# Performance work log

Measured on AMD Instinct MI355X. Metric: run time of the kernel, lower is better.

The kernel has to match this reference:

```python
import jax, jax.numpy as jnp
import numpy as np

A = 32          # num input capsule types
PSIZE = 16      # caps_size (pose matrix 4x4)
MD = 4          # mat_dim = sqrt(caps_size)
NCLS = 10       # output capsules / classes
KF = 5          # routing kernel (final_shape)
KK = KF * KF
KKA = KK * A
ITERS = 3
FINAL_LAMBDA = 0.01
EPS = 1e-12
LN2PI = float(np.log(2.0 * np.pi))
BN_EPS = 1e-5


def unfold(x, k, stride, pad):
    # torch.nn.functional.unfold: [b,C,h,w] -> [b, C*k*k, L], (c, kh, kw) channel-major
    b, c, h, w = x.shape
    if pad:
        x = jnp.pad(x, ((0, 0), (0, 0), (pad, pad), (pad, pad)))
    oh = (h + 2 * pad - k) // stride + 1
    ow = (w + 2 * pad - k) // stride + 1
    cols = jnp.stack([
        jnp.stack([x[:, :, i:i + stride * oh:stride, j:j + stride * ow:stride]
                   for j in range(k)], axis=3)
        for i in range(k)], axis=2)          # [b, c, k, k, oh, ow]
    return cols.reshape(b, c * k * k, oh * ow)


def conv3x3(x, w):
    return jax.lax.conv_general_dilated(x, w, (1, 1), [(1, 1), (1, 1)],
                                        dimension_numbers=('NCHW', 'OIHW', 'NCHW'))


def bn_inf(x, g, b, m, v):
    scale = g / jnp.sqrt(v + BN_EPS)
    return (x - m[None, :, None, None]) * scale[None, :, None, None] + b[None, :, None, None]


def em_routing(a_in, pose, W, beta_u, beta_a):
    b = a_in.shape[0]
    # pose votes
    pu = unfold(pose, KF, 1, 0)                     # [b, A*PSIZE*KK, l]
    l = pu.shape[-1]
    pu = pu.reshape(b, A, PSIZE, KK, l).transpose(0, 4, 3, 1, 2).reshape(b, l, KKA, PSIZE)
    pm = pu.reshape(b, l, KKA, MD, MD)[:, :, :, None]        # [b,l,kkA,1,md,md]
    v = jnp.matmul(pm, W)                                    # [b,l,kkA,B,md,md]
    v = v.reshape(b, l, KKA, NCLS, PSIZE)
    # activations
    au = unfold(a_in, KF, 1, 0).reshape(b, A, KK, l).transpose(0, 3, 2, 1).reshape(b, l, KKA)
    r = jnp.ones((b, l, KKA, NCLS, 1), v.dtype)
    a_out = mu = None
    for i in range(ITERS):
        lam = FINAL_LAMBDA * (1.0 - 0.95 ** (i + 1))
        # M-step
        rw = r * au[:, :, :, None, None]
        r_sum = rw.sum(axis=2, keepdims=True)                # [b,l,1,B,1]
        coeff = rw / (r_sum + EPS)
        mu = (coeff * v).sum(axis=2, keepdims=True)          # [b,l,1,B,psize]
        sigma_sq = (coeff * (v - mu) ** 2).sum(axis=2, keepdims=True) + EPS
        r_s = r_sum[:, :, 0]                                 # [b,l,B,1]
        sig = sigma_sq[:, :, 0]                              # [b,l,B,psize]
        cost_h = (beta_u + 0.5 * jnp.log(sig)) * r_s         # log(sqrt(s)) = 0.5*log(s)
        a_out = jax.nn.sigmoid(lam * (beta_a - cost_h.sum(axis=3)))   # [b,l,B]
        if i < ITERS - 1:
            # E-step (note: log(sigma_sq * ln2pi) as in original code)
            ln_p = (-0.5 * jnp.sum(jnp.log(sigma_sq * LN2PI), axis=-1)
                    - jnp.sum((v - mu) ** 2 / (2.0 * sigma_sq), axis=-1))   # [b,l,kkA,B]
            ln_ap = ln_p + jnp.log(a_out)[:, :, None, :]
            r = jax.nn.softmax(ln_ap, axis=-1)[..., None]
    oh = int(np.floor(np.sqrt(l)))
    pose_out = mu[:, :, 0].reshape(b, l, -1).transpose(0, 2, 1).reshape(b, -1, oh, oh)
    a_map = a_out.transpose(0, 2, 1).reshape(b, -1, oh, oh)
    return a_map, pose_out


def setup_inputs():
    key = jax.random.key(0)
    ks = jax.random.split(key, 14)
    batch = 256
    x = jax.random.normal(ks[0], (batch, 512, 5, 5), jnp.float32)
    w_a = jax.random.normal(ks[1], (A, 512, 3, 3), jnp.float32) * 0.02
    w_pose = jax.random.normal(ks[2], (A * PSIZE, 512, 3, 3), jnp.float32) * 0.02
    bn_a_g = 1.0 + 0.1 * jax.random.normal(ks[3], (A,), jnp.float32)
    bn_a_b = 0.1 * jax.random.normal(ks[4], (A,), jnp.float32)
    bn_a_m = 0.1 * jax.random.normal(ks[5], (A,), jnp.float32)
    bn_a_v = jax.random.uniform(ks[6], (A,), jnp.float32, 0.5, 1.5)
    C2 = A * PSIZE
    bn_p_g = 1.0 + 0.1 * jax.random.normal(ks[7], (C2,), jnp.float32)
    bn_p_b = 0.1 * jax.random.normal(ks[8], (C2,), jnp.float32)
    bn_p_m = 0.1 * jax.random.normal(ks[9], (C2,), jnp.float32)
    bn_p_v = jax.random.uniform(ks[10], (C2,), jnp.float32, 0.5, 1.5)
    W = jax.random.normal(ks[11], (KKA, NCLS, MD, MD), jnp.float32) * 0.25
    beta_u = jnp.zeros((1, 1, NCLS, 1), jnp.float32)
    beta_a = jnp.zeros((1, 1, NCLS), jnp.float32)
    return {"x": x, "w_a": w_a, "w_pose": w_pose,
            "bn_a_g": bn_a_g, "bn_a_b": bn_a_b, "bn_a_m": bn_a_m, "bn_a_v": bn_a_v,
            "bn_p_g": bn_p_g, "bn_p_b": bn_p_b, "bn_p_m": bn_p_m, "bn_p_v": bn_p_v,
            "W": W, "beta_u": beta_u, "beta_a": beta_a}


def reference(x, w_a, w_pose, bn_a_g, bn_a_b, bn_a_m, bn_a_v,
              bn_p_g, bn_p_b, bn_p_m, bn_p_v, W, beta_u, beta_a):
    a = jax.nn.sigmoid(bn_inf(conv3x3(x, w_a), bn_a_g, bn_a_b, bn_a_m, bn_a_v))
    pose = bn_inf(conv3x3(x, w_pose), bn_p_g, bn_p_b, bn_p_m, bn_p_v)
    a_map, _ = em_routing(a, pose, W, beta_u, beta_a)
    out = a_map.reshape(a_map.shape[0], -1)          # [b, 10]
    out = out / out.sum(axis=1, keepdims=True)
    return jnp.log(out)
```

## Files before the change

kernel.cpp:

```cpp
#include <hip/hip_runtime.h>
#include <math.h>

#define CIN 512
#define NCLS 10
#define KDIM 4608
#define NTOT 6400
#define MPAD 640
#define BK 128
#define NKT 36
#define NABLK (5 * NKT)
#define LN2PI_F 1.8378770664093453f

typedef __attribute__((ext_vector_type(8))) short bf16x8;
typedef __attribute__((ext_vector_type(4))) float f32x4;

typedef const __attribute__((address_space(1))) void* gas_ptr;
typedef __attribute__((address_space(3))) void* las_ptr;

__device__ __forceinline__ void async_copy16(const void* g, void* l) {
    __builtin_amdgcn_global_load_lds((gas_ptr)g, (las_ptr)l, 16, 0, 0);
}

__device__ __forceinline__ unsigned short f2bf(float f) {
    unsigned int u = __float_as_uint(f);
    u = (u + 0x7fffu + ((u >> 16) & 1u)) >> 16;
    return (unsigned short)u;
}
__device__ __forceinline__ float bf2f(unsigned short s) {
    return __uint_as_float(((unsigned int)s) << 16);
}
__device__ __forceinline__ float fexp(float x) { return __expf(x); }
__device__ __forceinline__ float flog(float x) { return __logf(x); }

__global__ __launch_bounds__(256) void pack_a_kernel(
    const float* __restrict__ w_pose, const float* __restrict__ w_a,
    const float* __restrict__ bn_p_g, const float* __restrict__ bn_p_b,
    const float* __restrict__ bn_p_m, const float* __restrict__ bn_p_v,
    const float* __restrict__ bn_a_g, const float* __restrict__ bn_a_b,
    const float* __restrict__ bn_a_m, const float* __restrict__ bn_a_v,
    const float* __restrict__ Wm,
    unsigned short* __restrict__ At, unsigned short* __restrict__ Wmb,
    float* __restrict__ sc, float* __restrict__ bi)
{
    const int blk = blockIdx.x;
    const int t = threadIdx.x;

    if (blk >= NABLK) {
        const int chunk = (blk - NABLK) * 256 + t;
        if (chunk < 16000) {
            const int e = chunk >> 1, half = chunk & 1;
            const int m = e / 10, c = e - m * 10;
            const int kk = m >> 5, a = m & 31;
            const int de = (kk * 10 + c) * 32 + a;
            const float4* s4 = reinterpret_cast<const float4*>(Wm + (size_t)chunk * 8);
            float4 x0 = s4[0], x1 = s4[1];
            int4 o;
            o.x = (int)f2bf(x0.x) | ((int)f2bf(x0.y) << 16);
            o.y = (int)f2bf(x0.z) | ((int)f2bf(x0.w) << 16);
            o.z = (int)f2bf(x1.x) | ((int)f2bf(x1.y) << 16);
            o.w = (int)f2bf(x1.z) | ((int)f2bf(x1.w) << 16);
            reinterpret_cast<int4*>(Wmb + ((size_t)de * 2 + half) * 8)[0] = o;
        }
        return;
    }

    const int mblk = blk / NKT;
    if (blk == 0) {
        for (int i = t; i < MPAD; i += 256) {
            float s = 0.f, b = 0.f;
            if (i < 512) {
                s = bn_p_g[i] / sqrtf(bn_p_v[i] + 1e-5f);
                b = bn_p_b[i] - bn_p_m[i] * s;
            } else if (i < 544) {
                const int j = i - 512;
                s = bn_a_g[j] / sqrtf(bn_a_v[j] + 1e-5f);
                b = bn_a_b[j] - bn_a_m[j] * s;
            }
            sc[i] = s; bi[i] = b;
        }
    }

    const int kt = blk - mblk * NKT;
    #pragma unroll
    for (int j = 0; j < 8; ++j) {
        const int c = t + j * 256;
        const int kc8 = c >> 7, slot = c & 127;
        const int row = mblk * 128 + (slot ^ (kc8 << 2));
        const int k0 = (kt * 16 + kc8) * 8;
        float v[8] = {0.f,0.f,0.f,0.f,0.f,0.f,0.f,0.f};
        if (row < 512) {
            const float4* s4 = reinterpret_cast<const float4*>(w_pose + (size_t)row * KDIM + k0);
            float4 x0 = s4[0], x1 = s4[1];
            v[0]=x0.x; v[1]=x0.y; v[2]=x0.z; v[3]=x0.w;
            v[4]=x1.x; v[5]=x1.y; v[6]=x1.z; v[7]=x1.w;
        } else if (row < 544) {
            const float4* s4 = reinterpret_cast<const float4*>(w_a + (size_t)(row - 512) * KDIM + k0);
            float4 x0 = s4[0], x1 = s4[1];
            v[0]=x0.x; v[1]=x0.y; v[2]=x0.z; v[3]=x0.w;
            v[4]=x1.x; v[5]=x1.y; v[6]=x1.z; v[7]=x1.w;
        }
        int4 o;
        o.x = (int)f2bf(v[0]) | ((int)f2bf(v[1]) << 16);
        o.y = (int)f2bf(v[2]) | ((int)f2bf(v[3]) << 16);
        o.z = (int)f2bf(v[4]) | ((int)f2bf(v[5]) << 16);
        o.w = (int)f2bf(v[6]) | ((int)f2bf(v[7]) << 16);
        reinterpret_cast<int4*>(At + ((((size_t)blk) << 11) + c) * 8)[0] = o;
    }
}

__global__ __launch_bounds__(1024) void pack_b_kernel(
    const float* __restrict__ x, unsigned short* __restrict__ Bt)
{
    __shared__ __align__(16) float xs[CIN * 25];
    const int b = blockIdx.x;
    const int t = threadIdx.x;
    const float4* xb = reinterpret_cast<const float4*>(x + (size_t)b * (CIN * 25));
    for (int f4 = t; f4 < (CIN * 25) / 4; f4 += 1024)
        reinterpret_cast<float4*>(xs)[f4] = xb[f4];
    __syncthreads();

    for (int w = t; w < 25 * (KDIM / 8); w += 1024) {
        const int ch = w / 25;
        const int px = w - ch * 25;
        const int py = px / 5, qx = px % 5;
        const int k0 = ch * 8;
        unsigned short v[8];
        #pragma unroll
        for (int j = 0; j < 8; ++j) {
            const int k = k0 + j;
            const int ci = k / 9;
            const int kk = k - ci * 9;
            const int dy = kk / 3, dx = kk - dy * 3;
            const int yy = py + dy - 1, xx = qx + dx - 1;
            const bool ok = (yy >= 0) & (yy < 5) & (xx >= 0) & (xx < 5);
            v[j] = ok ? f2bf(xs[ci * 25 + yy * 5 + xx]) : (unsigned short)0;
        }
        int4 o;
        o.x = (int)v[0] | ((int)v[1] << 16);
        o.y = (int)v[2] | ((int)v[3] << 16);
        o.z = (int)v[4] | ((int)v[5] << 16);
        o.w = (int)v[6] | ((int)v[7] << 16);
        const int n = b * 25 + px;
        const int nblk = n >> 7, nr = n & 127;
        const int kt = k0 >> 7;
        const int kc8 = (k0 >> 3) & 15;
        const int c = kc8 * 128 + (nr ^ (kc8 << 2));
        reinterpret_cast<int4*>(Bt + ((((size_t)(nblk * NKT + kt)) << 11) + c) * 8)[0] = o;
    }
}

__global__ __launch_bounds__(1024) void gemm_kernel(
    const unsigned short* __restrict__ At,
    const unsigned short* __restrict__ Bt,
    const float* __restrict__ sc, const float* __restrict__ bi,
    unsigned short* __restrict__ Cp,
    float* __restrict__ Ca)
{
    __shared__ __align__(16) unsigned char smem[131072];
    const int t = threadIdx.x;
    const int L = blockIdx.x;
    int mblk, nblk;
    if (L >= 240) { const int i = L - 240; mblk = i >> 1; nblk = 48 + (i & 1); }
    else          { const int q = L / 40, r = L - q * 40;
                    mblk = r >> 3; nblk = q * 8 + (r & 7); }
    const int m0 = mblk * 128, n0 = nblk * 128;
    const int lane = t & 63, w = t >> 6;
    const int g = w >> 2, wq = w & 3;
    const int wm = wq >> 1, wn = wq & 1;
    const int row16 = lane & 15, quad = lane >> 4;

    f32x4 acc[4][4] = {};

    const unsigned short* gAbase = At + (((size_t)mblk * NKT) << 14);
    const unsigned short* gBbase = Bt + (((size_t)nblk * NKT) << 14);

    #define STAGE(kt, s)                                                      \
    {                                                                         \
        unsigned short* As_ = (unsigned short*)(smem + (s) * 65536);          \
        unsigned short* Bs_ = As_ + 16384;                                    \
        const unsigned short* ga = gAbase + ((size_t)(kt) << 14);             \
        const unsigned short* gb = gBbase + ((size_t)(kt) << 14);             \
        _Pragma("unroll")                                                     \
        for (int j = 0; j < 2; ++j) {                                         \
            async_copy16(ga + ((size_t)(j * 1024 + t) << 3),                  \
                         As_ + ((size_t)(j * 1024 + w * 64) << 3));           \
            async_copy16(gb + ((size_t)(j * 1024 + t) << 3),                  \
                         Bs_ + ((size_t)(j * 1024 + w * 64) << 3));           \
        }                                                                     \
    }

    #define COMPUTE(s)                                                        \
    {                                                                         \
        const unsigned short* As_ = (const unsigned short*)(smem + (s) * 65536);\
        const unsigned short* Bs_ = As_ + 16384;                              \
        const int kc8b = g * 4 + quad;                                        \
        const int sw = kc8b << 2;                                             \
        bf16x8 af[4], bfr[4];                                                 \
        _Pragma("unroll")                                                     \
        for (int mt = 0; mt < 4; ++mt)                                        \
            af[mt] = *reinterpret_cast<const bf16x8*>(                        \
                &As_[(size_t)(kc8b * 128 + ((wm * 64 + mt * 16 + row16) ^ sw)) * 8]);\
        _Pragma("unroll")                                                     \
        for (int nt = 0; nt < 4; ++nt)                                        \
            bfr[nt] = *reinterpret_cast<const bf16x8*>(                       \
                &Bs_[(size_t)(kc8b * 128 + ((wn * 64 + nt * 16 + row16) ^ sw)) * 8]);\
        _Pragma("unroll")                                                     \
        for (int mt = 0; mt < 4; ++mt)                                        \
            _Pragma("unroll")                                                 \
            for (int nt = 0; nt < 4; ++nt)                                    \
                acc[mt][nt] = __builtin_amdgcn_mfma_f32_16x16x32_bf16(        \
                    af[mt], bfr[nt], acc[mt][nt], 0, 0, 0);                   \
    }

    STAGE(0, 0);
    for (int kt = 0; kt < NKT; ++kt) {
        __syncthreads();
        if (kt + 1 < NKT) STAGE(kt + 1, (kt + 1) & 1);
        COMPUTE(kt & 1);
    }
    #undef STAGE
    #undef COMPUTE

    f32x4* mb = (f32x4*)smem;
    #pragma unroll
    for (int r = 1; r < 4; ++r) {
        __syncthreads();
        if (g == r) {
            f32x4* dst = mb + wq * 1024;
            #pragma unroll
            for (int i = 0; i < 16; ++i)
                dst[i * 64 + lane] = acc[i >> 2][i & 3];
        }
        __syncthreads();
        if (g == 0) {
            const f32x4* src = mb + wq * 1024;
            #pragma unroll
            for (int i = 0; i < 16; ++i)
                acc[i >> 2][i & 3] += src[i * 64 + lane];
        }
    }

    if (g == 0) {
        #pragma unroll
        for (int mt = 0; mt < 4; ++mt) {
            const int mbase = m0 + wm * 64 + mt * 16 + quad * 4;
            if (mbase >= 544) continue;
            #pragma unroll
            for (int rg = 0; rg < 4; ++rg) {
                const int m = mbase + rg;
                const float s = sc[m], bbx = bi[m];
                #pragma unroll
                for (int nt = 0; nt < 4; ++nt) {
                    const int n = n0 + wn * 64 + nt * 16 + row16;
                    const float v = fmaf(acc[mt][nt][rg], s, bbx);
                    if (m < 512) Cp[(size_t)m * NTOT + n] = f2bf(v);
                    else Ca[(size_t)(m - 512) * NTOT + n] = 1.f / (1.f + fexp(-v));
                }
            }
        }
    }
}

__global__ __launch_bounds__(640, 1) void em_kernel(
    const unsigned short* __restrict__ Cp,
    const float* __restrict__ Ca,
    const unsigned short* __restrict__ Wmb,
    const float* __restrict__ beta_u, const float* __restrict__ beta_a,
    float* __restrict__ out)
{
    __shared__ __align__(16) float psh[25][32][20];
    __shared__ float aush[800];
    __shared__ float lnqp[2][NCLS][800];
    __shared__ float mu_sh[NCLS][16];
    __shared__ float i2s_sh[NCLS][16];
    __shared__ float costp[2][NCLS];
    __shared__ float slgp[2][NCLS];
    __shared__ float Kc_sh[NCLS];
    __shared__ float aout_sh[NCLS];

    const int b = blockIdx.x, t = threadIdx.x;
    const int rh = (t >= 320) ? 1 : 0;
    const int th = t - rh * 320;
    const int c = th >> 5, a = th & 31;
    float* rwsh = &lnqp[1][0][0];

    const unsigned short* pb = Cp + (size_t)b * 25;
    for (int f = t; f < 12800; f += 640) {
        const int c2 = f / 25, px = f - c2 * 25;
        psh[px][c2 >> 4][c2 & 15] = bf2f(pb[(size_t)c2 * NTOT + px]);
    }
    const float* ab = Ca + (size_t)b * 25;
    for (int f = t; f < 800; f += 640) {
        const int ci = f / 25, px = f - ci * 25;
        aush[px * 32 + ci] = ab[(size_t)ci * NTOT + px];
    }
    __syncthreads();

    const float bu = beta_u[c], ba = beta_a[c];
    float muL[8], i2sL[8], KcL = 0.f;
    const unsigned short* wbase = Wmb + ((size_t)(c * 32 + a)) * 16;

    #define UNPACK_VOTE(w0_, w1_, kk_, vv)                                   \
        {                                                                    \
            float pm[8], wv[16];                                             \
            const float4* pr = reinterpret_cast<const float4*>(&psh[kk_][a][rh * 8]); \
            const float4 p0 = pr[0], p1 = pr[1];                             \
            pm[0]=p0.x; pm[1]=p0.y; pm[2]=p0.z; pm[3]=p0.w;                  \
            pm[4]=p1.x; pm[5]=p1.y; pm[6]=p1.z; pm[7]=p1.w;                  \
            const unsigned int uu[8] = {(unsigned)w0_.x,(unsigned)w0_.y,     \
                (unsigned)w0_.z,(unsigned)w0_.w,(unsigned)w1_.x,             \
                (unsigned)w1_.y,(unsigned)w1_.z,(unsigned)w1_.w};            \
            _Pragma("unroll")                                                \
            for (int i = 0; i < 8; ++i) {                                    \
                wv[2*i]   = __uint_as_float(uu[i] << 16);                    \
                wv[2*i+1] = __uint_as_float(uu[i] & 0xFFFF0000u);            \
            }                                                                \
            _Pragma("unroll")                                                \
            for (int jr = 0; jr < 2; ++jr) {                                 \
                _Pragma("unroll")                                            \
                for (int s = 0; s < 4; ++s) {                                \
                    float av = 0.f;                                          \
                    _Pragma("unroll")                                        \
                    for (int tt = 0; tt < 4; ++tt)                           \
                        av = fmaf(pm[jr*4+tt], wv[tt*4+s], av);              \
                    vv[jr*4+s] = av;                                         \
                }                                                            \
            }                                                                \
        }

    float p95 = 1.f;
    for (int it = 0; it < 3; ++it) {
        p95 *= 0.95f;
        const float lam = 0.01f * (1.f - p95);

        if (it > 0) {
            int4 wr0 = *reinterpret_cast<const int4*>(wbase);
            int4 wr1 = *reinterpret_cast<const int4*>(wbase + 8);
            for (int kk = 0; kk < 25; ++kk) {
                const int4 w0 = wr0, w1 = wr1;
                if (kk < 24) {
                    const unsigned short* wn = wbase + (size_t)(kk + 1) * 5120;
                    wr0 = *reinterpret_cast<const int4*>(wn);
                    wr1 = *reinterpret_cast<const int4*>(wn + 8);
                }
                float vv[8];
                UNPACK_VOTE(w0, w1, kk, vv);
                float q = (rh == 0) ? KcL : 0.f;
                #pragma unroll
                for (int j = 0; j < 8; ++j) {
                    const float d = vv[j] - muL[j];
                    q -= d * d * i2sL[j];
                }
                lnqp[rh][c][kk * 32 + a] = q;
            }
            __syncthreads();
            {
                float* l0 = &lnqp[0][0][0];
                const float* l1 = &lnqp[1][0][0];
                for (int f = t; f < 8000; f += 640) l0[f] += l1[f];
            }
            __syncthreads();
            {
                const int k0 = rh ? 13 : 0, k1 = rh ? 25 : 13;
                for (int kk = k0; kk < k1; ++kk) {
                    const int m = kk * 32 + a;
                    float qv[NCLS];
                    #pragma unroll
                    for (int cc = 0; cc < NCLS; ++cc) qv[cc] = lnqp[0][cc][m];
                    float mx = qv[0];
                    #pragma unroll
                    for (int cc = 1; cc < NCLS; ++cc) mx = fmaxf(mx, qv[cc]);
                    float den = 0.f;
                    #pragma unroll
                    for (int cc = 0; cc < NCLS; ++cc) den += fexp(qv[cc] - mx);
                    rwsh[c * 800 + m] = fexp(qv[c] - mx) * __builtin_amdgcn_rcpf(den)
                                        * aush[m];
                }
            }
            __syncthreads();
        }

        float S0 = 0.f, S1[8], S2[8];
        #pragma unroll
        for (int j = 0; j < 8; ++j) { S1[j] = 0.f; S2[j] = 0.f; }

        int4 wA0 = *reinterpret_cast<const int4*>(wbase);
        int4 wA1 = *reinterpret_cast<const int4*>(wbase + 8);
        int4 wB0 = *reinterpret_cast<const int4*>(wbase + 5120);
        int4 wB1 = *reinterpret_cast<const int4*>(wbase + 5120 + 8);
        for (int kk = 0; kk < 25; ++kk) {
            const int4 w0 = wA0, w1 = wA1;
            wA0 = wB0; wA1 = wB1;
            if (kk < 23) {
                const unsigned short* wn = wbase + (size_t)(kk + 2) * 5120;
                wB0 = *reinterpret_cast<const int4*>(wn);
                wB1 = *reinterpret_cast<const int4*>(wn + 8);
            }
            float vv[8];
            UNPACK_VOTE(w0, w1, kk, vv);
            const int m = kk * 32 + a;
            const float rw = (it == 0) ? aush[m] : rwsh[c * 800 + m];
            S0 += rw;
            #pragma unroll
            for (int j = 0; j < 8; ++j) {
                const float rv = rw * vv[j];
                S1[j] += rv;
                S2[j] = fmaf(rv, vv[j], S2[j]);
            }
        }

        #pragma unroll
        for (int off = 16; off >= 1; off >>= 1) {
            S0 += __shfl_xor(S0, off);
            #pragma unroll
            for (int j = 0; j < 8; ++j) {
                S1[j] += __shfl_xor(S1[j], off);
                S2[j] += __shfl_xor(S2[j], off);
            }
        }

        if (a == 0) {
            const float s0e = S0 + 1e-12f;
            const float inv = 1.f / s0e;
            float cost_ = 0.f, slg_ = 0.f;
            #pragma unroll
            for (int j = 0; j < 8; ++j) {
                const float mu_ = S1[j] * inv;
                const float sg = (S2[j] - 2.f * mu_ * S1[j] + mu_ * mu_ * S0) * inv
                                 + 1e-12f;
                cost_ += bu + 0.5f * flog(sg);
                slg_ += flog(sg * LN2PI_F);
                mu_sh[c][rh * 8 + j] = mu_;
                i2s_sh[c][rh * 8 + j] = 0.5f / sg;
            }
            costp[rh][c] = cost_;
            slgp[rh][c] = slg_;
        }
        __syncthreads();
        if (a == 0 && rh == 0) {
            const float costsum = (costp[0][c] + costp[1][c]) * S0;
            const float aout = 1.f / (1.f + fexp(-(lam * (ba - costsum))));
            aout_sh[c] = aout;
            Kc_sh[c] = flog(aout) - 0.5f * (slgp[0][c] + slgp[1][c]);
        }
        __syncthreads();
        if (it < 2) {
            #pragma unroll
            for (int j = 0; j < 8; ++j) {
                muL[j] = mu_sh[c][rh * 8 + j];
                i2sL[j] = i2s_sh[c][rh * 8 + j];
            }
            KcL = Kc_sh[c];
        }
    }

    if (t < NCLS) {
        float s = 0.f;
        #pragma unroll
        for (int cc = 0; cc < NCLS; ++cc) s += aout_sh[cc];
        out[b * NCLS + t] = flog(aout_sh[t] / s);
    }
    #undef UNPACK_VOTE
}

extern "C" void kernel_launch(void* const* d_in, const int* in_sizes, int n_in,
                              void* d_out, int out_size, void* d_ws, size_t ws_size,
                              hipStream_t stream) {
    const float* x      = (const float*)d_in[0];
    const float* w_a    = (const float*)d_in[1];
    const float* w_pose = (const float*)d_in[2];
    const float* bn_a_g = (const float*)d_in[3];
    const float* bn_a_b = (const float*)d_in[4];
    const float* bn_a_m = (const float*)d_in[5];
    const float* bn_a_v = (const float*)d_in[6];
    const float* bn_p_g = (const float*)d_in[7];
    const float* bn_p_b = (const float*)d_in[8];
    const float* bn_p_m = (const float*)d_in[9];
    const float* bn_p_v = (const float*)d_in[10];
    const float* Wm     = (const float*)d_in[11];
    const float* beta_u = (const float*)d_in[12];
    const float* beta_a = (const float*)d_in[13];
    float* out = (float*)d_out;

    char* p = (char*)d_ws;
    unsigned short* At  = (unsigned short*)p;  p += (size_t)MPAD * KDIM * 2;
    unsigned short* Bt  = (unsigned short*)p;  p += (size_t)NTOT * KDIM * 2;
    unsigned short* Wmb = (unsigned short*)p;  p += (size_t)800 * NCLS * 16 * 2;
    unsigned short* Cp  = (unsigned short*)p;  p += (size_t)512 * NTOT * 2;
    float* Ca = (float*)p;                     p += (size_t)32 * NTOT * 4;
    float* sc = (float*)p;                     p += MPAD * 4;
    float* bi = (float*)p;                     p += MPAD * 4;

    pack_a_kernel<<<NABLK + 63, 256, 0, stream>>>(w_pose, w_a,
                                                  bn_p_g, bn_p_b, bn_p_m, bn_p_v,
                                                  bn_a_g, bn_a_b, bn_a_m, bn_a_v,
                                                  Wm, At, Wmb, sc, bi);
    pack_b_kernel<<<256, 1024, 0, stream>>>(x, Bt);
    gemm_kernel<<<250, 1024, 0, stream>>>(At, Bt, sc, bi, Cp, Ca);
    em_kernel<<<256, 640, 0, stream>>>(Cp, Ca, Wmb, beta_u, beta_a, out);
}
```

Before: 231.6 us.

## Split EM routing kernel positions across three thread groups with cross-group reduction

The EM routing kernel grows from 640 to 960 threads. The 25 kernel positions are split into three groups, and each thread processes two input capsule types. Partial M-step sums are reduced through shared memory before the statistics are computed. The E-step softmax is restructured so that each of 800 threads handles one position for all classes, instead of recomputing the max and denominator per class. This adds parallelism and removes redundant softmax work, at the cost of an extra barrier and partial-sum traffic, plus register pressure from the larger block.

```diff
diff --git a/kernel.cpp b/kernel.cpp
--- a/kernel.cpp
+++ b/kernel.cpp
@@ -261,7 +261,7 @@
     }
 }
 
-__global__ __launch_bounds__(640, 1) void em_kernel(
+__global__ __launch_bounds__(960) void em_kernel(
     const unsigned short* __restrict__ Cp,
     const float* __restrict__ Ca,
     const unsigned short* __restrict__ Wmb,
@@ -277,20 +277,24 @@
     __shared__ float slgp[2][NCLS];
     __shared__ float Kc_sh[NCLS];
     __shared__ float aout_sh[NCLS];
+    __shared__ float part[3][2][NCLS][17];
 
     const int b = blockIdx.x, t = threadIdx.x;
-    const int rh = (t >= 320) ? 1 : 0;
-    const int th = t - rh * 320;
-    const int c = th >> 5, a = th & 31;
+    const int g3 = t / 320;
+    const int th = t - g3 * 320;
+    const int rh = th / 160;
+    const int th2 = th - rh * 160;
+    const int c = th2 >> 4, a = th2 & 15;
+    const int klo = g3 * 8, khi = (g3 == 2) ? 25 : (g3 * 8 + 8);
     float* rwsh = &lnqp[1][0][0];
 
     const unsigned short* pb = Cp + (size_t)b * 25;
-    for (int f = t; f < 12800; f += 640) {
+    for (int f = t; f < 12800; f += 960) {
         const int c2 = f / 25, px = f - c2 * 25;
         psh[px][c2 >> 4][c2 & 15] = bf2f(pb[(size_t)c2 * NTOT + px]);
     }
     const float* ab = Ca + (size_t)b * 25;
-    for (int f = t; f < 800; f += 640) {
+    for (int f = t; f < 800; f += 960) {
         const int ci = f / 25, px = f - ci * 25;
         aush[px * 32 + ci] = ab[(size_t)ci * NTOT + px];
     }
@@ -298,12 +302,13 @@
 
     const float bu = beta_u[c], ba = beta_a[c];
     float muL[8], i2sL[8], KcL = 0.f;
-    const unsigned short* wbase = Wmb + ((size_t)(c * 32 + a)) * 16;
-
-    #define UNPACK_VOTE(w0_, w1_, kk_, vv)                                   \
+    const unsigned short* wb0 = Wmb + ((size_t)(c * 32 + a)) * 16;
+    const unsigned short* wb1 = Wmb + ((size_t)(c * 32 + a + 16)) * 16;
+
+    #define UNPACK_VOTE(w0_, w1_, kk_, av_, vv)                              \
         {                                                                    \
             float pm[8], wv[16];                                             \
-            const float4* pr = reinterpret_cast<const float4*>(&psh[kk_][a][rh * 8]); \
+            const float4* pr = reinterpret_cast<const float4*>(&psh[kk_][av_][rh * 8]); \
             const float4 p0 = pr[0], p1 = pr[1];                             \
             pm[0]=p0.x; pm[1]=p0.y; pm[2]=p0.z; pm[3]=p0.w;                  \
             pm[4]=p1.x; pm[5]=p1.y; pm[6]=p1.z; pm[7]=p1.w;                  \
@@ -319,63 +324,77 @@
             for (int jr = 0; jr < 2; ++jr) {                                 \
                 _Pragma("unroll")                                            \
                 for (int s = 0; s < 4; ++s) {                                \
-                    float av = 0.f;                                          \
+                    float sacc = 0.f;                                        \
                     _Pragma("unroll")                                        \
                     for (int tt = 0; tt < 4; ++tt)                           \
-                        av = fmaf(pm[jr*4+tt], wv[tt*4+s], av);              \
-                    vv[jr*4+s] = av;                                         \
+                        sacc = fmaf(pm[jr*4+tt], wv[tt*4+s], sacc);          \
+                    vv[jr*4+s] = sacc;                                       \
                 }                                                            \
             }                                                                \
         }
 
+    float T0 = 0.f;
     float p95 = 1.f;
     for (int it = 0; it < 3; ++it) {
         p95 *= 0.95f;
         const float lam = 0.01f * (1.f - p95);
 
         if (it > 0) {
-            int4 wr0 = *reinterpret_cast<const int4*>(wbase);
-            int4 wr1 = *reinterpret_cast<const int4*>(wbase + 8);
-            for (int kk = 0; kk < 25; ++kk) {
-                const int4 w0 = wr0, w1 = wr1;
-                if (kk < 24) {
-                    const unsigned short* wn = wbase + (size_t)(kk + 1) * 5120;
-                    wr0 = *reinterpret_cast<const int4*>(wn);
-                    wr1 = *reinterpret_cast<const int4*>(wn + 8);
+            int4 a00 = *reinterpret_cast<const int4*>(wb0 + (size_t)klo * 5120);
+            int4 a01 = *reinterpret_cast<const int4*>(wb0 + (size_t)klo * 5120 + 8);
+            int4 a10 = *reinterpret_cast<const int4*>(wb1 + (size_t)klo * 5120);
+            int4 a11 = *reinterpret_cast<const int4*>(wb1 + (size_t)klo * 5120 + 8);
+            for (int kk = klo; kk < khi; ++kk) {
+                const int4 w00 = a00, w01 = a01, w10 = a10, w11 = a11;
+                if (kk + 1 < khi) {
+                    const unsigned short* n0 = wb0 + (size_t)(kk + 1) * 5120;
+                    const unsigned short* n1 = wb1 + (size_t)(kk + 1) * 5120;
+                    a00 = *reinterpret_cast<const int4*>(n0);
+                    a01 = *reinterpret_cast<const int4*>(n0 + 8);
+                    a10 = *reinterpret_cast<const int4*>(n1);
+                    a11 = *reinterpret_cast<const int4*>(n1 + 8);
                 }
-                float vv[8];
-                UNPACK_VOTE(w0, w1, kk, vv);
-                float q = (rh == 0) ? KcL : 0.f;
+                float vv0[8], vv1[8];
+                UNPACK_VOTE(w00, w01, kk, a, vv0);
+                UNPACK_VOTE(w10, w11, kk, a + 16, vv1);
+                float q0 = (rh == 0) ? KcL : 0.f;
+                float q1 = q0;
                 #pragma unroll
                 for (int j = 0; j < 8; ++j) {
-                    const float d = vv[j] - muL[j];
-                    q -= d * d * i2sL[j];
+                    const float d0 = vv0[j] - muL[j];
+                    q0 -= d0 * d0 * i2sL[j];
+                    const float d1 = vv1[j] - muL[j];
+                    q1 -= d1 * d1 * i2sL[j];
                 }
-                lnqp[rh][c][kk * 32 + a] = q;
+                lnqp[rh][c][kk * 32 + a] = q0;
+                lnqp[rh][c][kk * 32 + a + 16] = q1;
             }
             __syncthreads();
             {
                 float* l0 = &lnqp[0][0][0];
                 const float* l1 = &lnqp[1][0][0];
-                for (int f = t; f < 8000; f += 640) l0[f] += l1[f];
+                for (int f = t; f < 8000; f += 960) l0[f] += l1[f];
             }
             __syncthreads();
-            {
-                const int k0 = rh ? 13 : 0, k1 = rh ? 25 : 13;
-                for (int kk = k0; kk < k1; ++kk) {
-                    const int m = kk * 32 + a;
-                    float qv[NCLS];
-                    #pragma unroll
-                    for (int cc = 0; cc < NCLS; ++cc) qv[cc] = lnqp[0][cc][m];
-                    float mx = qv[0];
-                    #pragma unroll
-                    for (int cc = 1; cc < NCLS; ++cc) mx = fmaxf(mx, qv[cc]);
-                    float den = 0.f;
-                    #pragma unroll
-                    for (int cc = 0; cc < NCLS; ++cc) den += fexp(qv[cc] - mx);
-                    rwsh[c * 800 + m] = fexp(qv[c] - mx) * __builtin_amdgcn_rcpf(den)
-                                        * aush[m];
+            if (t < 800) {
+                const int m = t;
+                float qv[NCLS];
+                #pragma unroll
+                for (int cc = 0; cc < NCLS; ++cc) qv[cc] = lnqp[0][cc][m];
+                float mx = qv[0];
+                #pragma unroll
+                for (int cc = 1; cc < NCLS; ++cc) mx = fmaxf(mx, qv[cc]);
+                float ev[NCLS];
+                float den = 0.f;
+                #pragma unroll
+                for (int cc = 0; cc < NCLS; ++cc) {
+                    ev[cc] = fexp(qv[cc] - mx);
+                    den += ev[cc];
                 }
+                const float s = aush[m] * __builtin_amdgcn_rcpf(den);
+                #pragma unroll
+                for (int cc = 0; cc < NCLS; ++cc)
+                    rwsh[cc * 800 + m] = ev[cc] * s;
             }
             __syncthreads();
         }
@@ -384,33 +403,38 @@
         #pragma unroll
         for (int j = 0; j < 8; ++j) { S1[j] = 0.f; S2[j] = 0.f; }
 
-        int4 wA0 = *reinterpret_cast<const int4*>(wbase);
-        int4 wA1 = *reinterpret_cast<const int4*>(wbase + 8);
-        int4 wB0 = *reinterpret_cast<const int4*>(wbase + 5120);
-        int4 wB1 = *reinterpret_cast<const int4*>(wbase + 5120 + 8);
-        for (int kk = 0; kk < 25; ++kk) {
-            const int4 w0 = wA0, w1 = wA1;
-            wA0 = wB0; wA1 = wB1;
-            if (kk < 23) {
-                const unsigned short* wn = wbase + (size_t)(kk + 2) * 5120;
-                wB0 = *reinterpret_cast<const int4*>(wn);
-                wB1 = *reinterpret_cast<const int4*>(wn + 8);
-            }
-            float vv[8];
-            UNPACK_VOTE(w0, w1, kk, vv);
-            const int m = kk * 32 + a;
-            const float rw = (it == 0) ? aush[m] : rwsh[c * 800 + m];
-            S0 += rw;
+        int4 a00 = *reinterpret_cast<const int4*>(wb0 + (size_t)klo * 5120);
+        int4 a01 = *reinterpret_cast<const int4*>(wb0 + (size_t)klo * 5120 + 8);
+        int4 a10 = *reinterpret_cast<const int4*>(wb1 + (size_t)klo * 5120);
+        int4 a11 = *reinterpret_cast<const int4*>(wb1 + (size_t)klo * 5120 + 8);
+        for (int kk = klo; kk < khi; ++kk) {
+            const int4 w00 = a00, w01 = a01, w10 = a10, w11 = a11;
+            if (kk + 1 < khi) {
+                const unsigned short* n0 = wb0 + (size_t)(kk + 1) * 5120;
+                const unsigned short* n1 = wb1 + (size_t)(kk + 1) * 5120;
+                a00 = *reinterpret_cast<const int4*>(n0);
+                a01 = *reinterpret_cast<const int4*>(n0 + 8);
+                a10 = *reinterpret_cast<const int4*>(n1);
+                a11 = *reinterpret_cast<const int4*>(n1 + 8);
+            }
+            float vv0[8], vv1[8];
+            UNPACK_VOTE(w00, w01, kk, a, vv0);
+            UNPACK_VOTE(w10, w11, kk, a + 16, vv1);
+            const int m0 = kk * 32 + a, m1 = m0 + 16;
+            const float rw0 = (it == 0) ? aush[m0] : rwsh[c * 800 + m0];
+            const float rw1 = (it == 0) ? aush[m1] : rwsh[c * 800 + m1];
+            S0 += rw0 + rw1;
             #pragma unroll
             for (int j = 0; j < 8; ++j) {
-                const float rv = rw * vv[j];
-                S1[j] += rv;
-                S2[j] = fmaf(rv, vv[j], S2[j]);
+                const float rv0 = rw0 * vv0[j];
+                const float rv1 = rw1 * vv1[j];
+                S1[j] += rv0 + rv1;
+                S2[j] = fmaf(rv0, vv0[j], fmaf(rv1, vv1[j], S2[j]));
             }
         }
 
         #pragma unroll
-        for (int off = 16; off >= 1; off >>= 1) {
+        for (int off = 8; off >= 1; off >>= 1) {
             S0 += __shfl_xor(S0, off);
             #pragma unroll
             for (int j = 0; j < 8; ++j) {
@@ -420,13 +444,29 @@
         }
 
         if (a == 0) {
-            const float s0e = S0 + 1e-12f;
+            float* pp = part[g3][rh][c];
+            pp[0] = S0;
+            #pragma unroll
+            for (int j = 0; j < 8; ++j) { pp[1 + j] = S1[j]; pp[9 + j] = S2[j]; }
+        }
+        __syncthreads();
+        if (g3 == 0 && a == 0) {
+            T0 = part[0][rh][c][0] + part[1][rh][c][0] + part[2][rh][c][0];
+            float T1[8], T2[8];
+            #pragma unroll
+            for (int j = 0; j < 8; ++j) {
+                T1[j] = part[0][rh][c][1 + j] + part[1][rh][c][1 + j]
+                      + part[2][rh][c][1 + j];
+                T2[j] = part[0][rh][c][9 + j] + part[1][rh][c][9 + j]
+                      + part[2][rh][c][9 + j];
+            }
+            const float s0e = T0 + 1e-12f;
             const float inv = 1.f / s0e;
             float cost_ = 0.f, slg_ = 0.f;
             #pragma unroll
             for (int j = 0; j < 8; ++j) {
-                const float mu_ = S1[j] * inv;
-                const float sg = (S2[j] - 2.f * mu_ * S1[j] + mu_ * mu_ * S0) * inv
+                const float mu_ = T1[j] * inv;
+                const float sg = (T2[j] - 2.f * mu_ * T1[j] + mu_ * mu_ * T0) * inv
                                  + 1e-12f;
                 cost_ += bu + 0.5f * flog(sg);
                 slg_ += flog(sg * LN2PI_F);
@@ -437,8 +477,8 @@
             slgp[rh][c] = slg_;
         }
         __syncthreads();
-        if (a == 0 && rh == 0) {
-            const float costsum = (costp[0][c] + costp[1][c]) * S0;
+        if (g3 == 0 && a == 0 && rh == 0) {
+            const float costsum = (costp[0][c] + costp[1][c]) * T0;
             const float aout = 1.f / (1.f + fexp(-(lam * (ba - costsum))));
             aout_sh[c] = aout;
             Kc_sh[c] = flog(aout) - 0.5f * (slgp[0][c] + slgp[1][c]);
@@ -497,5 +537,5 @@
                                                   Wm, At, Wmb, sc, bi);
     pack_b_kernel<<<256, 1024, 0, stream>>>(x, Bt);
     gemm_kernel<<<250, 1024, 0, stream>>>(At, Bt, sc, bi, Cp, Ca);
-    em_kernel<<<256, 640, 0, stream>>>(Cp, Ca, Wmb, beta_u, beta_a, out);
-}
+    em_kernel<<<256, 960, 0, stream>>>(Cp, Ca, Wmb, beta_u, beta_a, out);
+}
```

Result: slower. 260.8 us (+12.6%).

## Remap EM threads so pose halves share a wave and merge softmax pass

Applied to the files above, without the earlier changes.

Thread mapping changes so the two 8-element pose halves of one class sit in the same wave. The lnq partial sums are then combined with a cross-lane shuffle instead of a second LDS buffer plus an extra add pass and barrier. Pose data stays bf16 in LDS in a vector-friendly layout and is prefetched one step ahead. The softmax pass now computes all classes per position in a single loop. This cuts LDS footprint, one barrier and a full LDS add pass, at the cost of extra unpack work and an unevenly distributed softmax loop (800 positions over 640 threads).

```diff
diff --git a/kernel.cpp b/kernel.cpp
--- a/kernel.cpp
+++ b/kernel.cpp
@@ -268,9 +268,9 @@
     const float* __restrict__ beta_u, const float* __restrict__ beta_a,
     float* __restrict__ out)
 {
-    __shared__ __align__(16) float psh[25][32][20];
+    __shared__ __align__(16) unsigned short psh[25][2][32][8];
     __shared__ float aush[800];
-    __shared__ float lnqp[2][NCLS][800];
+    __shared__ float lnq[NCLS][800];
     __shared__ float mu_sh[NCLS][16];
     __shared__ float i2s_sh[NCLS][16];
     __shared__ float costp[2][NCLS];
@@ -279,15 +279,15 @@
     __shared__ float aout_sh[NCLS];
 
     const int b = blockIdx.x, t = threadIdx.x;
-    const int rh = (t >= 320) ? 1 : 0;
-    const int th = t - rh * 320;
-    const int c = th >> 5, a = th & 31;
-    float* rwsh = &lnqp[1][0][0];
+    const int c = t >> 6;
+    const int rh = (t >> 5) & 1;
+    const int a = t & 31;
 
     const unsigned short* pb = Cp + (size_t)b * 25;
     for (int f = t; f < 12800; f += 640) {
         const int c2 = f / 25, px = f - c2 * 25;
-        psh[px][c2 >> 4][c2 & 15] = bf2f(pb[(size_t)c2 * NTOT + px]);
+        const int e = c2 & 15;
+        psh[px][e >> 3][c2 >> 4][e & 7] = pb[(size_t)c2 * NTOT + px];
     }
     const float* ab = Ca + (size_t)b * 25;
     for (int f = t; f < 800; f += 640) {
@@ -300,13 +300,16 @@
     float muL[8], i2sL[8], KcL = 0.f;
     const unsigned short* wbase = Wmb + ((size_t)(c * 32 + a)) * 16;
 
-    #define UNPACK_VOTE(w0_, w1_, kk_, vv)                                   \
+    #define VOTE(w0_, w1_, p_, vv)                                           \
         {                                                                    \
             float pm[8], wv[16];                                             \
-            const float4* pr = reinterpret_cast<const float4*>(&psh[kk_][a][rh * 8]); \
-            const float4 p0 = pr[0], p1 = pr[1];                             \
-            pm[0]=p0.x; pm[1]=p0.y; pm[2]=p0.z; pm[3]=p0.w;                  \
-            pm[4]=p1.x; pm[5]=p1.y; pm[6]=p1.z; pm[7]=p1.w;                  \
+            const unsigned int pu[4] = {(unsigned)p_.x, (unsigned)p_.y,      \
+                                        (unsigned)p_.z, (unsigned)p_.w};     \
+            _Pragma("unroll")                                                \
+            for (int i = 0; i < 4; ++i) {                                    \
+                pm[2*i]   = __uint_as_float(pu[i] << 16);                    \
+                pm[2*i+1] = __uint_as_float(pu[i] & 0xFFFF0000u);            \
+            }                                                                \
             const unsigned int uu[8] = {(unsigned)w0_.x,(unsigned)w0_.y,     \
                 (unsigned)w0_.z,(unsigned)w0_.w,(unsigned)w1_.x,             \
                 (unsigned)w1_.y,(unsigned)w1_.z,(unsigned)w1_.w};            \
@@ -336,46 +339,45 @@
         if (it > 0) {
             int4 wr0 = *reinterpret_cast<const int4*>(wbase);
             int4 wr1 = *reinterpret_cast<const int4*>(wbase + 8);
+            int4 pr  = *reinterpret_cast<const int4*>(&psh[0][rh][a][0]);
             for (int kk = 0; kk < 25; ++kk) {
-                const int4 w0 = wr0, w1 = wr1;
+                const int4 w0 = wr0, w1 = wr1, p = pr;
                 if (kk < 24) {
                     const unsigned short* wn = wbase + (size_t)(kk + 1) * 5120;
                     wr0 = *reinterpret_cast<const int4*>(wn);
                     wr1 = *reinterpret_cast<const int4*>(wn + 8);
+                    pr  = *reinterpret_cast<const int4*>(&psh[kk + 1][rh][a][0]);
                 }
                 float vv[8];
-                UNPACK_VOTE(w0, w1, kk, vv);
+                VOTE(w0, w1, p, vv);
                 float q = (rh == 0) ? KcL : 0.f;
                 #pragma unroll
                 for (int j = 0; j < 8; ++j) {
                     const float d = vv[j] - muL[j];
                     q -= d * d * i2sL[j];
                 }
-                lnqp[rh][c][kk * 32 + a] = q;
+                q += __shfl_xor(q, 32);
+                if (rh == 0) lnq[c][kk * 32 + a] = q;
             }
             __syncthreads();
-            {
-                float* l0 = &lnqp[0][0][0];
-                const float* l1 = &lnqp[1][0][0];
-                for (int f = t; f < 8000; f += 640) l0[f] += l1[f];
-            }
-            __syncthreads();
-            {
-                const int k0 = rh ? 13 : 0, k1 = rh ? 25 : 13;
-                for (int kk = k0; kk < k1; ++kk) {
-                    const int m = kk * 32 + a;
-                    float qv[NCLS];
-                    #pragma unroll
-                    for (int cc = 0; cc < NCLS; ++cc) qv[cc] = lnqp[0][cc][m];
-                    float mx = qv[0];
-                    #pragma unroll
-                    for (int cc = 1; cc < NCLS; ++cc) mx = fmaxf(mx, qv[cc]);
-                    float den = 0.f;
-                    #pragma unroll
-                    for (int cc = 0; cc < NCLS; ++cc) den += fexp(qv[cc] - mx);
-                    rwsh[c * 800 + m] = fexp(qv[c] - mx) * __builtin_amdgcn_rcpf(den)
-                                        * aush[m];
+            for (int m = t; m < 800; m += 640) {
+                float qv[NCLS];
+                #pragma unroll
+                for (int cc = 0; cc < NCLS; ++cc) qv[cc] = lnq[cc][m];
+                float mx = qv[0];
+                #pragma unroll
+                for (int cc = 1; cc < NCLS; ++cc) mx = fmaxf(mx, qv[cc]);
+                float ev[NCLS];
+                float den = 0.f;
+                #pragma unroll
+                for (int cc = 0; cc < NCLS; ++cc) {
+                    ev[cc] = fexp(qv[cc] - mx);
+                    den += ev[cc];
                 }
+                const float s = aush[m] * __builtin_amdgcn_rcpf(den);
+                #pragma unroll
+                for (int cc = 0; cc < NCLS; ++cc)
+                    lnq[cc][m] = ev[cc] * s;
             }
             __syncthreads();
         }
@@ -388,18 +390,21 @@
         int4 wA1 = *reinterpret_cast<const int4*>(wbase + 8);
         int4 wB0 = *reinterpret_cast<const int4*>(wbase + 5120);
         int4 wB1 = *reinterpret_cast<const int4*>(wbase + 5120 + 8);
+        int4 pr  = *reinterpret_cast<const int4*>(&psh[0][rh][a][0]);
         for (int kk = 0; kk < 25; ++kk) {
-            const int4 w0 = wA0, w1 = wA1;
+            const int4 w0 = wA0, w1 = wA1, p = pr;
             wA0 = wB0; wA1 = wB1;
             if (kk < 23) {
                 const unsigned short* wn = wbase + (size_t)(kk + 2) * 5120;
                 wB0 = *reinterpret_cast<const int4*>(wn);
                 wB1 = *reinterpret_cast<const int4*>(wn + 8);
             }
+            if (kk < 24)
+                pr = *reinterpret_cast<const int4*>(&psh[kk + 1][rh][a][0]);
             float vv[8];
-            UNPACK_VOTE(w0, w1, kk, vv);
+            VOTE(w0, w1, p, vv);
             const int m = kk * 32 + a;
-            const float rw = (it == 0) ? aush[m] : rwsh[c * 800 + m];
+            const float rw = (it == 0) ? aush[m] : lnq[c][m];
             S0 += rw;
             #pragma unroll
             for (int j = 0; j < 8; ++j) {
@@ -460,7 +465,7 @@
         for (int cc = 0; cc < NCLS; ++cc) s += aout_sh[cc];
         out[b * NCLS + t] = flog(aout_sh[t] / s);
     }
-    #undef UNPACK_VOTE
+    #undef VOTE
 }
 
 extern "C" void kernel_launch(void* const* d_in, const int* in_sizes, int n_in,
```

After: 227.0 us (median of 3 runs). -2.0%, faster.
